# Kernel tuning notes

Hardware: AMD Instinct MI355X
Metric: run time of the kernel (lower is better)

The kernel has to match this reference:

```python
import jax, jax.numpy as jnp
import numpy as np

N_NODES = 100000


def _gcn_layer(x, W, b, src, dst, n):
    # PyG GCNConv with default add_self_loops=True, symmetric normalization.
    h = x @ W  # [N, out]
    deg = jax.ops.segment_sum(jnp.ones_like(dst, dtype=h.dtype), dst, num_segments=n)
    dinv = jnp.where(deg > 0, jax.lax.rsqrt(deg), 0.0)
    norm = dinv[src] * dinv[dst]  # [E]
    msg = h[src] * norm[:, None]  # gather + scale
    out = jax.ops.segment_sum(msg, dst, num_segments=n)  # scatter-add at targets
    return out + b


def setup_inputs() -> dict:
    key = jax.random.key(0)
    ks = jax.random.split(key, 8)
    n, e = N_NODES, 3200000
    x = jax.random.normal(ks[0], (n, 16), dtype=jnp.float32)
    edge_index = jax.random.randint(ks[1], (2, e), 0, n, dtype=jnp.int64)
    def glorot(k, fi, fo):
        lim = float(np.sqrt(6.0 / (fi + fo)))
        return jax.random.uniform(k, (fi, fo), jnp.float32, -lim, lim)
    return {
        "x": x,
        "edge_index": edge_index,
        "W1": glorot(ks[2], 16, 32), "b1": jnp.zeros((32,), jnp.float32),
        "W2": glorot(ks[3], 32, 64), "b2": jnp.zeros((64,), jnp.float32),
        "W3": glorot(ks[4], 64, 1),  "b3": jnp.zeros((1,), jnp.float32),
    }


def reference(x, edge_index, W1, b1, W2, b2, W3, b3):
    n = x.shape[0]
    # add self-loops once (shared by all layers)
    loops = jnp.arange(n, dtype=edge_index.dtype)
    src = jnp.concatenate([edge_index[0], loops])
    dst = jnp.concatenate([edge_index[1], loops])
    h = _gcn_layer(x, W1, b1, src, dst, n)
    h = jax.nn.relu(h)  # dropout is identity in eval mode
    h = _gcn_layer(h, W2, b2, src, dst, n)
    h = jax.nn.relu(h)
    h = _gcn_layer(h, W3, b3, src, dst, n)
    return jax.nn.sigmoid(h)
```

## Files before the change

kernel.cpp:

```cpp
#include <hip/hip_runtime.h>
#include <hip/hip_bf16.h>
#include <math.h>


#define CW    512
#define CSH   9
#define MAXBUKC 256
#define EPB   8192
#define CAP   24576

static inline int cdiv(int a, int b) { return (a + b - 1) / b; }

__device__ inline unsigned int bf16_rn(float f) {
    unsigned int u = __float_as_uint(f);
    return (u + 0x7fffu + ((u >> 16) & 1u)) >> 16;
}
#define BLO(u) __uint_as_float((u) << 16)
#define BHI(u) __uint_as_float((u) & 0xffff0000u)

#define UNPACK_ADD(A, V) \
    A[0] += BLO(V.x); A[1] += BHI(V.x); \
    A[2] += BLO(V.y); A[3] += BHI(V.y); \
    A[4] += BLO(V.z); A[5] += BHI(V.z); \
    A[6] += BLO(V.w); A[7] += BHI(V.w);


__global__ void __launch_bounds__(256) k_bscatter(const int* __restrict__ src,
                                                  const int* __restrict__ dst,
                                                  int* __restrict__ gcur,
                                                  int* __restrict__ ebuf, int e, int nbuk) {
    __shared__ int lh[MAXBUKC];
    __shared__ int lo[MAXBUKC];
    __shared__ int lb[MAXBUKC];
    __shared__ int sh[256];
    __shared__ int stage[EPB];
    __shared__ unsigned char bkOf[EPB];
    int4 db[8];
    int t = threadIdx.x;
    for (int b = t; b < nbuk; b += 256) lh[b] = 0;
    __syncthreads();
    int base4 = blockIdx.x * (EPB / 4);
    int e4 = e >> 2;
#pragma unroll
    for (int j = 0; j < 8; j++) {
        int i4 = base4 + j * 256 + t;
        if (i4 < e4) {
            int4 d = ((const int4*)dst)[i4];
            db[j] = d;
            atomicAdd(&lh[d.x >> CSH], 1); atomicAdd(&lh[d.y >> CSH], 1);
            atomicAdd(&lh[d.z >> CSH], 1); atomicAdd(&lh[d.w >> CSH], 1);
        } else db[j] = make_int4(-1, -1, -1, -1);
    }
    __syncthreads();
    int c = (t < nbuk) ? lh[t] : 0;
    int gb = (t < nbuk && c) ? (t * CAP + atomicAdd(&gcur[t], c)) : 0;
    sh[t] = c;
    __syncthreads();
    for (int o = 1; o < 256; o <<= 1) {
        int u = (t >= o) ? sh[t - o] : 0;
        __syncthreads();
        sh[t] += u;
        __syncthreads();
    }
    if (t < nbuk) { lo[t] = sh[t] - c; lb[t] = gb; lh[t] = 0; }
    __syncthreads();
#pragma unroll
    for (int j = 0; j < 8; j++) {
        int i4 = base4 + j * 256 + t;
        if (i4 < e4) {
            int4 s = ((const int4*)src)[i4];
            int4 d = db[j];
            int dd, ss, b, r, slot;
#define PUT(DX, SX) \
            dd = DX; ss = SX; b = dd >> CSH; \
            r = atomicAdd(&lh[b], 1); slot = lo[b] + r; \
            stage[slot] = ((dd & (CW - 1)) << 17) | ss; \
            bkOf[slot] = (unsigned char)b;
            PUT(d.x, s.x) PUT(d.y, s.y) PUT(d.z, s.z) PUT(d.w, s.w)
#undef PUT
        }
    }
    __syncthreads();
    int tot = min(EPB, e - blockIdx.x * EPB);
#pragma unroll
    for (int j = 0; j < 32; j++) {
        int slot = j * 256 + t;
        if (slot < tot) {
            int b = bkOf[slot];
            ebuf[lb[b] + (slot - lo[b])] = stage[slot];
        }
    }
}


__global__ void __launch_bounds__(256) k_bscan(const int* __restrict__ gcur,
                                               int* __restrict__ boffD,
                                               int nbuk, int e) {
    __shared__ int sh[256];
    int t = threadIdx.x;
    int v = (t < nbuk) ? gcur[t] : 0;
    sh[t] = v;
    __syncthreads();
    for (int o = 1; o < 256; o <<= 1) {
        int u = (t >= o) ? sh[t - o] : 0;
        __syncthreads();
        sh[t] += u;
        __syncthreads();
    }
    if (t < nbuk) boffD[t] = sh[t] - v;
    if (t == 0) boffD[nbuk] = e;
}


__global__ void __launch_bounds__(1024) k_csr2(const int* __restrict__ ebuf,
                                               const int* __restrict__ bcnt,
                                               const int* __restrict__ boffD,
                                               int* __restrict__ rowstart,
                                               int* __restrict__ csr_src,
                                               float* __restrict__ dinv,
                                               const float* __restrict__ x,
                                               unsigned int* __restrict__ xs,
                                               int n, int e) {
    __shared__ int cnt[CW];
    __shared__ int offs[CW];
    int t = threadIdx.x;
    if (t < CW) cnt[t] = 0;
    __syncthreads();
    int cnt_b = bcnt[blockIdx.x];
    int dbeg = boffD[blockIdx.x];
    const int4* eb4 = (const int4*)(ebuf + (size_t)blockIdx.x * CAP);
    int n4 = (cnt_b + 3) >> 2;
    for (int k4 = t; k4 < n4; k4 += 1024) {
        int4 v = eb4[k4];
        int rem = cnt_b - (k4 << 2);
        atomicAdd(&cnt[v.x >> 17], 1);
        if (rem > 1) atomicAdd(&cnt[v.y >> 17], 1);
        if (rem > 2) atomicAdd(&cnt[v.z >> 17], 1);
        if (rem > 3) atomicAdd(&cnt[v.w >> 17], 1);
    }
    __syncthreads();
    int v = (t < CW) ? cnt[t] : 0;
    if (t < CW) offs[t] = v;
    __syncthreads();
    for (int o = 1; o < CW; o <<= 1) {
        int u = (t < CW && t >= o) ? offs[t - o] : 0;
        __syncthreads();
        if (t < CW) offs[t] += u;
        __syncthreads();
    }
    int node = blockIdx.x * CW + t;
    if (t < CW) {
        int ex = offs[t] - v;
        float dd = rsqrtf((float)v + 1.0f);
        if (node < n) {
            rowstart[node] = dbeg + ex;
            dinv[node] = dd;
            const float4* xr = (const float4*)(x + (size_t)node * 16);
            float4 v0 = xr[0], v1 = xr[1], v2 = xr[2], v3 = xr[3];
            uint4 o0, o1;
            o0.x = bf16_rn(v0.x * dd) | (bf16_rn(v0.y * dd) << 16);
            o0.y = bf16_rn(v0.z * dd) | (bf16_rn(v0.w * dd) << 16);
            o0.z = bf16_rn(v1.x * dd) | (bf16_rn(v1.y * dd) << 16);
            o0.w = bf16_rn(v1.z * dd) | (bf16_rn(v1.w * dd) << 16);
            o1.x = bf16_rn(v2.x * dd) | (bf16_rn(v2.y * dd) << 16);
            o1.y = bf16_rn(v2.z * dd) | (bf16_rn(v2.w * dd) << 16);
            o1.z = bf16_rn(v3.x * dd) | (bf16_rn(v3.y * dd) << 16);
            o1.w = bf16_rn(v3.z * dd) | (bf16_rn(v3.w * dd) << 16);
            uint4* xo = (uint4*)(xs + (size_t)node * 8);
            xo[0] = o0; xo[1] = o1;
        }
        cnt[t] = ex;
    }
    __syncthreads();
    for (int k4 = t; k4 < n4; k4 += 1024) {
        int4 vv = eb4[k4];
        int rem = cnt_b - (k4 << 2);
        int pv, r;
#define SCAT(PV) pv = PV; r = atomicAdd(&cnt[pv >> 17], 1); csr_src[dbeg + r] = pv & 0x1FFFF;
        SCAT(vv.x)
        if (rem > 1) { SCAT(vv.y) }
        if (rem > 2) { SCAT(vv.z) }
        if (rem > 3) { SCAT(vv.w) }
#undef SCAT
    }
    if (blockIdx.x == 0 && t == 0) rowstart[n] = e;
}


__global__ void __launch_bounds__(256) k_pull16(const int* __restrict__ rowstart,
                                                const int* __restrict__ csr_src,
                                                const float* __restrict__ dinv,
                                                const unsigned int* __restrict__ xs,
                                                float* __restrict__ agg16, int n) {
    int wid = (blockIdx.x * blockDim.x + threadIdx.x) >> 6;
    if (wid >= n) return;
    int lane = threadIdx.x & 63;
    int half = lane & 1;
    int beg = rowstart[wid], end = rowstart[wid + 1];
    const uint4* x4 = (const uint4*)xs;
    float dd = dinv[wid];
    uint4 sv = x4[(size_t)wid * 2 + half];
    float acc[8], ac1[8];
#pragma unroll
    for (int i = 0; i < 8; i++) { acc[i] = 0.f; ac1[i] = 0.f; }
    int k = beg + (lane >> 1);
    for (; k + 32 < end; k += 64) {
        int s0 = __builtin_nontemporal_load(csr_src + k);
        int s1 = __builtin_nontemporal_load(csr_src + k + 32);
        uint4 v0 = x4[(size_t)s0 * 2 + half];
        uint4 v1 = x4[(size_t)s1 * 2 + half];
        UNPACK_ADD(acc, v0);
        UNPACK_ADD(ac1, v1);
    }
    if (k < end) {
        int s0 = __builtin_nontemporal_load(csr_src + k);
        uint4 v0 = x4[(size_t)s0 * 2 + half];
        UNPACK_ADD(acc, v0);
    }
#pragma unroll
    for (int i = 0; i < 8; i++) acc[i] += ac1[i];
#pragma unroll
    for (int off = 2; off < 64; off <<= 1)
#pragma unroll
        for (int i = 0; i < 8; i++) acc[i] += __shfl_xor(acc[i], off);
    UNPACK_ADD(acc, sv);
    if (lane < 2) {
        float4* o4 = (float4*)(agg16 + (size_t)wid * 16 + half * 8);
        o4[0] = make_float4(acc[0] * dd, acc[1] * dd, acc[2] * dd, acc[3] * dd);
        o4[1] = make_float4(acc[4] * dd, acc[5] * dd, acc[6] * dd, acc[7] * dd);
    }
}


__global__ void __launch_bounds__(256) k_dense1(const float* __restrict__ agg,
                                                const float* __restrict__ dinv,
                                                const float* __restrict__ W1,
                                                const float* __restrict__ b1,
                                                unsigned int* __restrict__ h1s, int n) {
    int node = blockIdx.x * 256 + threadIdx.x;
    if (node >= n) return;
    float dd = dinv[node];
    float in[16];
    const float4* a4 = (const float4*)(agg + (size_t)node * 16);
#pragma unroll
    for (int f = 0; f < 4; f++) {
        float4 v = a4[f];
        in[4 * f] = v.x; in[4 * f + 1] = v.y; in[4 * f + 2] = v.z; in[4 * f + 3] = v.w;
    }
    unsigned int hw[16];
#pragma unroll
    for (int c = 0; c < 16; c++) {
        float o0 = b1[2 * c], o1 = b1[2 * c + 1];
#pragma unroll
        for (int k = 0; k < 16; k++) {
            o0 += in[k] * W1[k * 32 + 2 * c];
            o1 += in[k] * W1[k * 32 + 2 * c + 1];
        }
        hw[c] = bf16_rn(fmaxf(o0, 0.f) * dd) | (bf16_rn(fmaxf(o1, 0.f) * dd) << 16);
    }
    uint4* o4 = (uint4*)(h1s + (size_t)node * 16);
    o4[0] = make_uint4(hw[0], hw[1], hw[2], hw[3]);
    o4[1] = make_uint4(hw[4], hw[5], hw[6], hw[7]);
    o4[2] = make_uint4(hw[8], hw[9], hw[10], hw[11]);
    o4[3] = make_uint4(hw[12], hw[13], hw[14], hw[15]);
}


__global__ void __launch_bounds__(256) k_pull32(const int* __restrict__ rowstart,
                                                const int* __restrict__ csr_src,
                                                const float* __restrict__ dinv,
                                                const unsigned int* __restrict__ h1s,
                                                float* __restrict__ agg32, int n) {
    int wid = (blockIdx.x * blockDim.x + threadIdx.x) >> 6;
    if (wid >= n) return;
    int lane = threadIdx.x & 63;
    int f4 = lane & 3;
    int beg = rowstart[wid], end = rowstart[wid + 1];
    const uint4* h4 = (const uint4*)h1s;
    float dd = dinv[wid];
    uint4 sv = h4[(size_t)wid * 4 + f4];
    float acc[8], ac1[8];
#pragma unroll
    for (int i = 0; i < 8; i++) { acc[i] = 0.f; ac1[i] = 0.f; }
    int k = beg + (lane >> 2);
    for (; k + 16 < end; k += 32) {
        int s0 = __builtin_nontemporal_load(csr_src + k);
        int s1 = __builtin_nontemporal_load(csr_src + k + 16);
        uint4 v0 = h4[(size_t)s0 * 4 + f4];
        uint4 v1 = h4[(size_t)s1 * 4 + f4];
        UNPACK_ADD(acc, v0);
        UNPACK_ADD(ac1, v1);
    }
    if (k < end) {
        int s0 = __builtin_nontemporal_load(csr_src + k);
        uint4 v0 = h4[(size_t)s0 * 4 + f4];
        UNPACK_ADD(acc, v0);
    }
#pragma unroll
    for (int i = 0; i < 8; i++) acc[i] += ac1[i];
#pragma unroll
    for (int off = 4; off < 64; off <<= 1)
#pragma unroll
        for (int i = 0; i < 8; i++) acc[i] += __shfl_xor(acc[i], off);
    UNPACK_ADD(acc, sv);
    if (lane < 4) {
        float4* o4 = (float4*)(agg32 + (size_t)wid * 32 + f4 * 8);
        o4[0] = make_float4(acc[0] * dd, acc[1] * dd, acc[2] * dd, acc[3] * dd);
        o4[1] = make_float4(acc[4] * dd, acc[5] * dd, acc[6] * dd, acc[7] * dd);
    }
}


__global__ void __launch_bounds__(256) k_dense2(const float* __restrict__ agg,
                                                const float* __restrict__ dinv,
                                                const float* __restrict__ W2,
                                                const float* __restrict__ b2,
                                                const float* __restrict__ W3,
                                                float* __restrict__ t2, int n) {
    int node = blockIdx.x * 256 + threadIdx.x;
    if (node >= n) return;
    float in[32];
    const float4* a4 = (const float4*)(agg + (size_t)node * 32);
#pragma unroll
    for (int f = 0; f < 8; f++) {
        float4 v = a4[f];
        in[4 * f] = v.x; in[4 * f + 1] = v.y; in[4 * f + 2] = v.z; in[4 * f + 3] = v.w;
    }
    float p = 0.f;
#pragma unroll
    for (int cb = 0; cb < 4; cb++) {
        float o[16];
#pragma unroll
        for (int c = 0; c < 16; c++) o[c] = b2[cb * 16 + c];
#pragma unroll
        for (int k = 0; k < 32; k++) {
            float ik = in[k];
#pragma unroll
            for (int c = 0; c < 16; c++) o[c] += ik * W2[k * 64 + cb * 16 + c];
        }
#pragma unroll
        for (int c = 0; c < 16; c++) p += fmaxf(o[c], 0.f) * W3[cb * 16 + c];
    }
    t2[node] = p * dinv[node];
}


__global__ void __launch_bounds__(256) k_pull1_sig(const int* __restrict__ rowstart,
                                                   const int* __restrict__ csr_src,
                                                   const float* __restrict__ dinv,
                                                   const float* __restrict__ t2,
                                                   const float* __restrict__ b3,
                                                   float* __restrict__ out, int n) {
    int tid = blockIdx.x * blockDim.x + threadIdx.x;
    int wid = tid >> 5;
    if (wid >= n) return;
    int lane32 = threadIdx.x & 31;
    int beg = rowstart[wid], end = rowstart[wid + 1];
    float selfv = t2[wid];
    float dd = dinv[wid];
    float acc = 0.f;
    for (int k = beg + lane32; k < end; k += 32)
        acc += t2[__builtin_nontemporal_load(csr_src + k)];
#pragma unroll
    for (int off = 1; off < 32; off <<= 1) acc += __shfl_xor(acc, off);
    if (lane32 == 0) {
        float v = (acc + selfv) * dd + b3[0];
        out[wid] = 1.0f / (1.0f + expf(-v));
    }
}


extern "C" void kernel_launch(void* const* d_in, const int* in_sizes, int n_in,
                              void* d_out, int out_size, void* d_ws, size_t ws_size,
                              hipStream_t stream) {
    const float* x  = (const float*)d_in[0];
    const int*   ei = (const int*)d_in[1];
    const float* W1 = (const float*)d_in[2];
    const float* b1 = (const float*)d_in[3];
    const float* W2 = (const float*)d_in[4];
    const float* b2 = (const float*)d_in[5];
    const float* W3 = (const float*)d_in[6];
    const float* b3 = (const float*)d_in[7];

    const int n = in_sizes[0] / 16;
    const int e = in_sizes[1] / 2;
    const int* src = ei;
    const int* dst = ei + e;
    const int nbuk = cdiv(n, CW);

    auto rup = [](size_t v) { return (v + 15) & ~(size_t)15; };
    char* wp = (char*)d_ws;
    auto alloc = [&](size_t elems) { void* p = wp; wp += rup(elems) * 4; return p; };
    int*   gcur     = (int*)  alloc(MAXBUKC);
    int*   boffD    = (int*)  alloc(MAXBUKC + 1);
    float* dinv     = (float*)alloc(n);
    int*   rowstart = (int*)  alloc(n + 1);
    int*   ebuf     = (int*)  alloc((size_t)nbuk * CAP);
    int*   csr_src  = (int*)  alloc(e);
    unsigned int* xs  = (unsigned int*)alloc((size_t)8 * n);
    unsigned int* h1s = (unsigned int*)alloc((size_t)16 * n);
    float* agg16    = (float*)alloc((size_t)16 * n);
    float* agg32    = (float*)alloc((size_t)32 * n);
    float* t2       = (float*)alloc(n);

    float* out = (float*)d_out;
    const int B = 256;
    const int pullGrid = cdiv(n * 64, B);

    hipMemsetAsync(gcur, 0, MAXBUKC * 4, stream);
    k_bscatter<<<cdiv(e, EPB), B, 0, stream>>>(src, dst, gcur, ebuf, e, nbuk);
    k_bscan<<<1, 256, 0, stream>>>(gcur, boffD, nbuk, e);
    k_csr2<<<nbuk, 1024, 0, stream>>>(ebuf, gcur, boffD, rowstart, csr_src,
                                      dinv, x, xs, n, e);

    k_pull16<<<pullGrid, B, 0, stream>>>(rowstart, csr_src, dinv, xs, agg16, n);
    k_dense1<<<cdiv(n, B), B, 0, stream>>>(agg16, dinv, W1, b1, h1s, n);

    k_pull32<<<pullGrid, B, 0, stream>>>(rowstart, csr_src, dinv, h1s, agg32, n);
    k_dense2<<<cdiv(n, B), B, 0, stream>>>(agg32, dinv, W2, b2, W3, t2, n);

    k_pull1_sig<<<cdiv(n * 32, B), B, 0, stream>>>(rowstart, csr_src, dinv, t2, b3, out, n);
}
```

Baseline: 224.0 us.

## Use finer CSR buckets, fold bucket scan into csr kernel, quad-lane pull16

Bucket width shrinks from 512 to 128 destination nodes, giving about four times as many CSR-build blocks with smaller capacity. The scatter kernel now scans bucket counts in chunks of 256. The separate bucket-offset scan kernel is removed; each csr block instead sums the preceding bucket counts itself. The first-layer pull now has four lanes per edge, each loading 8 bytes, so 16 edges are in flight per wave step instead of 32 lanes doing 16-byte loads. The aim is more parallelism in the CSR build and one fewer launch, at the cost of redundant prefix sums, more bucket atomics and a smaller per-bucket capacity margin.

```diff
diff --git a/kernel.cpp b/kernel.cpp
--- a/kernel.cpp
+++ b/kernel.cpp
@@ -3,11 +3,11 @@
 #include <math.h>
 
 
-#define CW    512
-#define CSH   9
-#define MAXBUKC 256
+#define CW    128
+#define CSH   7
+#define MAXBUK 1024
 #define EPB   8192
-#define CAP   24576
+#define CAP   5120
 
 static inline int cdiv(int a, int b) { return (a + b - 1) / b; }
 
@@ -23,18 +23,21 @@
     A[2] += BLO(V.y); A[3] += BHI(V.y); \
     A[4] += BLO(V.z); A[5] += BHI(V.z); \
     A[6] += BLO(V.w); A[7] += BHI(V.w);
+#define UNPACK_ADD2(A, V) \
+    A[0] += BLO(V.x); A[1] += BHI(V.x); \
+    A[2] += BLO(V.y); A[3] += BHI(V.y);
 
 
 __global__ void __launch_bounds__(256) k_bscatter(const int* __restrict__ src,
                                                   const int* __restrict__ dst,
                                                   int* __restrict__ gcur,
                                                   int* __restrict__ ebuf, int e, int nbuk) {
-    __shared__ int lh[MAXBUKC];
-    __shared__ int lo[MAXBUKC];
-    __shared__ int lb[MAXBUKC];
+    __shared__ int lh[MAXBUK];
+    __shared__ int lo[MAXBUK];
+    __shared__ int lb[MAXBUK];
     __shared__ int sh[256];
     __shared__ int stage[EPB];
-    __shared__ unsigned char bkOf[EPB];
+    __shared__ unsigned short bkOf[EPB];
     int4 db[8];
     int t = threadIdx.x;
     for (int b = t; b < nbuk; b += 256) lh[b] = 0;
@@ -52,17 +55,24 @@
         } else db[j] = make_int4(-1, -1, -1, -1);
     }
     __syncthreads();
-    int c = (t < nbuk) ? lh[t] : 0;
-    int gb = (t < nbuk && c) ? (t * CAP + atomicAdd(&gcur[t], c)) : 0;
-    sh[t] = c;
-    __syncthreads();
-    for (int o = 1; o < 256; o <<= 1) {
-        int u = (t >= o) ? sh[t - o] : 0;
+    int carry = 0;
+    for (int cb = 0; cb < nbuk; cb += 256) {
+        int b = cb + t;
+        int c = (b < nbuk) ? lh[b] : 0;
+        if (b < nbuk && c) lb[b] = b * CAP + atomicAdd(&gcur[b], c);
+        sh[t] = c;
         __syncthreads();
-        sh[t] += u;
+        for (int o = 1; o < 256; o <<= 1) {
+            int u = (t >= o) ? sh[t - o] : 0;
+            __syncthreads();
+            sh[t] += u;
+            __syncthreads();
+        }
+        if (b < nbuk) lo[b] = sh[t] - c + carry;
+        carry += sh[255];
         __syncthreads();
     }
-    if (t < nbuk) { lo[t] = sh[t] - c; lb[t] = gb; lh[t] = 0; }
+    for (int b = t; b < nbuk; b += 256) lh[b] = 0;
     __syncthreads();
 #pragma unroll
     for (int j = 0; j < 8; j++) {
@@ -75,7 +85,7 @@
             dd = DX; ss = SX; b = dd >> CSH; \
             r = atomicAdd(&lh[b], 1); slot = lo[b] + r; \
             stage[slot] = ((dd & (CW - 1)) << 17) | ss; \
-            bkOf[slot] = (unsigned char)b;
+            bkOf[slot] = (unsigned short)b;
             PUT(d.x, s.x) PUT(d.y, s.y) PUT(d.z, s.z) PUT(d.w, s.w)
 #undef PUT
         }
@@ -93,44 +103,34 @@
 }
 
 
-__global__ void __launch_bounds__(256) k_bscan(const int* __restrict__ gcur,
-                                               int* __restrict__ boffD,
-                                               int nbuk, int e) {
-    __shared__ int sh[256];
-    int t = threadIdx.x;
-    int v = (t < nbuk) ? gcur[t] : 0;
-    sh[t] = v;
-    __syncthreads();
-    for (int o = 1; o < 256; o <<= 1) {
-        int u = (t >= o) ? sh[t - o] : 0;
-        __syncthreads();
-        sh[t] += u;
-        __syncthreads();
-    }
-    if (t < nbuk) boffD[t] = sh[t] - v;
-    if (t == 0) boffD[nbuk] = e;
-}
-
-
-__global__ void __launch_bounds__(1024) k_csr2(const int* __restrict__ ebuf,
-                                               const int* __restrict__ bcnt,
-                                               const int* __restrict__ boffD,
-                                               int* __restrict__ rowstart,
-                                               int* __restrict__ csr_src,
-                                               float* __restrict__ dinv,
-                                               const float* __restrict__ x,
-                                               unsigned int* __restrict__ xs,
-                                               int n, int e) {
+__global__ void __launch_bounds__(512) k_csr2(const int* __restrict__ ebuf,
+                                              const int* __restrict__ gcur,
+                                              int* __restrict__ rowstart,
+                                              int* __restrict__ csr_src,
+                                              float* __restrict__ dinv,
+                                              const float* __restrict__ x,
+                                              unsigned int* __restrict__ xs,
+                                              int n, int e, int nbuk) {
     __shared__ int cnt[CW];
     __shared__ int offs[CW];
+    __shared__ int red[512];
     int t = threadIdx.x;
+    int bid = blockIdx.x;
+    int part = 0;
+    for (int j = t; j < bid; j += 512) part += gcur[j];
+    red[t] = part;
+    __syncthreads();
+    for (int o = 256; o > 0; o >>= 1) {
+        if (t < o) red[t] += red[t + o];
+        __syncthreads();
+    }
+    int dbeg = red[0];
     if (t < CW) cnt[t] = 0;
     __syncthreads();
-    int cnt_b = bcnt[blockIdx.x];
-    int dbeg = boffD[blockIdx.x];
-    const int4* eb4 = (const int4*)(ebuf + (size_t)blockIdx.x * CAP);
+    int cnt_b = gcur[bid];
+    const int4* eb4 = (const int4*)(ebuf + (size_t)bid * CAP);
     int n4 = (cnt_b + 3) >> 2;
-    for (int k4 = t; k4 < n4; k4 += 1024) {
+    for (int k4 = t; k4 < n4; k4 += 512) {
         int4 v = eb4[k4];
         int rem = cnt_b - (k4 << 2);
         atomicAdd(&cnt[v.x >> 17], 1);
@@ -148,7 +148,7 @@
         if (t < CW) offs[t] += u;
         __syncthreads();
     }
-    int node = blockIdx.x * CW + t;
+    int node = bid * CW + t;
     if (t < CW) {
         int ex = offs[t] - v;
         float dd = rsqrtf((float)v + 1.0f);
@@ -172,7 +172,7 @@
         cnt[t] = ex;
     }
     __syncthreads();
-    for (int k4 = t; k4 < n4; k4 += 1024) {
+    for (int k4 = t; k4 < n4; k4 += 512) {
         int4 vv = eb4[k4];
         int rem = cnt_b - (k4 << 2);
         int pv, r;
@@ -183,7 +183,7 @@
         if (rem > 3) { SCAT(vv.w) }
 #undef SCAT
     }
-    if (blockIdx.x == 0 && t == 0) rowstart[n] = e;
+    if (bid == 0 && t == 0) rowstart[n] = e;
 }
 
 
@@ -195,40 +195,38 @@
     int wid = (blockIdx.x * blockDim.x + threadIdx.x) >> 6;
     if (wid >= n) return;
     int lane = threadIdx.x & 63;
-    int half = lane & 1;
+    int q = lane & 3;
     int beg = rowstart[wid], end = rowstart[wid + 1];
-    const uint4* x4 = (const uint4*)xs;
+    const uint2* x2 = (const uint2*)xs;
     float dd = dinv[wid];
-    uint4 sv = x4[(size_t)wid * 2 + half];
-    float acc[8], ac1[8];
-#pragma unroll
-    for (int i = 0; i < 8; i++) { acc[i] = 0.f; ac1[i] = 0.f; }
-    int k = beg + (lane >> 1);
-    for (; k + 32 < end; k += 64) {
+    uint2 sv = x2[(size_t)wid * 4 + q];
+    float a0[4], a1[4];
+#pragma unroll
+    for (int i = 0; i < 4; i++) { a0[i] = 0.f; a1[i] = 0.f; }
+    int k = beg + (lane >> 2);
+    for (; k + 16 < end; k += 32) {
         int s0 = __builtin_nontemporal_load(csr_src + k);
-        int s1 = __builtin_nontemporal_load(csr_src + k + 32);
-        uint4 v0 = x4[(size_t)s0 * 2 + half];
-        uint4 v1 = x4[(size_t)s1 * 2 + half];
-        UNPACK_ADD(acc, v0);
-        UNPACK_ADD(ac1, v1);
+        int s1 = __builtin_nontemporal_load(csr_src + k + 16);
+        uint2 v0 = x2[(size_t)s0 * 4 + q];
+        uint2 v1 = x2[(size_t)s1 * 4 + q];
+        UNPACK_ADD2(a0, v0);
+        UNPACK_ADD2(a1, v1);
     }
     if (k < end) {
         int s0 = __builtin_nontemporal_load(csr_src + k);
-        uint4 v0 = x4[(size_t)s0 * 2 + half];
-        UNPACK_ADD(acc, v0);
-    }
-#pragma unroll
-    for (int i = 0; i < 8; i++) acc[i] += ac1[i];
-#pragma unroll
-    for (int off = 2; off < 64; off <<= 1)
-#pragma unroll
-        for (int i = 0; i < 8; i++) acc[i] += __shfl_xor(acc[i], off);
-    UNPACK_ADD(acc, sv);
-    if (lane < 2) {
-        float4* o4 = (float4*)(agg16 + (size_t)wid * 16 + half * 8);
-        o4[0] = make_float4(acc[0] * dd, acc[1] * dd, acc[2] * dd, acc[3] * dd);
-        o4[1] = make_float4(acc[4] * dd, acc[5] * dd, acc[6] * dd, acc[7] * dd);
-    }
+        uint2 v0 = x2[(size_t)s0 * 4 + q];
+        UNPACK_ADD2(a0, v0);
+    }
+#pragma unroll
+    for (int i = 0; i < 4; i++) a0[i] += a1[i];
+#pragma unroll
+    for (int off = 4; off < 64; off <<= 1)
+#pragma unroll
+        for (int i = 0; i < 4; i++) a0[i] += __shfl_xor(a0[i], off);
+    UNPACK_ADD2(a0, sv);
+    if (lane < 4)
+        ((float4*)(agg16 + (size_t)wid * 16))[q] =
+            make_float4(a0[0] * dd, a0[1] * dd, a0[2] * dd, a0[3] * dd);
 }
 
 
@@ -391,8 +389,7 @@
     auto rup = [](size_t v) { return (v + 15) & ~(size_t)15; };
     char* wp = (char*)d_ws;
     auto alloc = [&](size_t elems) { void* p = wp; wp += rup(elems) * 4; return p; };
-    int*   gcur     = (int*)  alloc(MAXBUKC);
-    int*   boffD    = (int*)  alloc(MAXBUKC + 1);
+    int*   gcur     = (int*)  alloc(MAXBUK);
     float* dinv     = (float*)alloc(n);
     int*   rowstart = (int*)  alloc(n + 1);
     int*   ebuf     = (int*)  alloc((size_t)nbuk * CAP);
@@ -407,11 +404,10 @@
     const int B = 256;
     const int pullGrid = cdiv(n * 64, B);
 
-    hipMemsetAsync(gcur, 0, MAXBUKC * 4, stream);
+    hipMemsetAsync(gcur, 0, MAXBUK * 4, stream);
     k_bscatter<<<cdiv(e, EPB), B, 0, stream>>>(src, dst, gcur, ebuf, e, nbuk);
-    k_bscan<<<1, 256, 0, stream>>>(gcur, boffD, nbuk, e);
-    k_csr2<<<nbuk, 1024, 0, stream>>>(ebuf, gcur, boffD, rowstart, csr_src,
-                                      dinv, x, xs, n, e);
+    k_csr2<<<nbuk, 512, 0, stream>>>(ebuf, gcur, rowstart, csr_src,
+                                     dinv, x, xs, n, e, nbuk);
 
     k_pull16<<<pullGrid, B, 0, stream>>>(rowstart, csr_src, dinv, xs, agg16, n);
     k_dense1<<<cdiv(n, B), B, 0, stream>>>(agg16, dinv, W1, b1, h1s, n);
```

Result: faster. 215.7 us (-3.7%).
